# Performance work log

Hardware: AMD Instinct MI355X
Metric: run time of the kernel (lower is better)

The kernel has to match this reference:

```python
import jax, jax.numpy as jnp
import numpy as np

DELTA = 5.0  # HuberLoss delta from the torch module


def setup_inputs() -> dict:
    key = jax.random.key(0)
    k1, k2 = jax.random.split(key)
    shape = (8, 1, 160, 160, 160)
    return {
        "y_pred_logits": jax.random.normal(k1, shape, dtype=jnp.float32),
        "y_true": jax.random.normal(k2, shape, dtype=jnp.float32),
    }


def reference(y_pred_logits, y_true):
    bs = y_true.shape[0]
    pred = y_pred_logits.astype(jnp.float32).reshape(bs, -1)
    true = y_true.astype(jnp.float32).reshape(bs, -1)
    e = pred - true
    ae = jnp.abs(e)
    # per-sample mean losses (matches per-iteration nn.MSELoss / L1Loss / HuberLoss)
    L2 = jnp.mean(e * e, axis=1)
    L1 = jnp.mean(ae, axis=1)
    huber_elem = jnp.where(ae <= DELTA, 0.5 * e * e, DELTA * (ae - 0.5 * DELTA))
    huber = jnp.mean(huber_elem, axis=1)
    # branch logic: L2 if (L2 <= 1) or (L2 > 1 and L2 < L1**2), else huber
    use_l2 = (L2 <= 1.0) | (L2 < L1 * L1)
    per_sample = jnp.where(use_l2, L2, huber)
    return jnp.mean(per_sample)
```

## Files before the change

### kernel.cpp

```cpp
#include <hip/hip_runtime.h>


#define TPB 256
#define BPS 500
constexpr int    F4_PER_SAMPLE = 1024000;
constexpr int    F4_PER_BLOCK  = 2048;
constexpr double PER_SAMPLE_D  = 4096000.0;
constexpr float  DELTA = 5.0f;

typedef float vf4 __attribute__((ext_vector_type(4)));

__global__ __launch_bounds__(TPB, 4) void adap_stage1(
    const vf4* __restrict__ pred,
    const vf4* __restrict__ truth,
    float* __restrict__ part)
{
    const int s   = blockIdx.y;
    const int b   = blockIdx.x;
    const int tid = threadIdx.x;
    const int base = s * F4_PER_SAMPLE + b * F4_PER_BLOCK + tid;

    vf4 p[8], t[8];
    #pragma unroll
    for (int j = 0; j < 8; ++j) {
        p[j] = pred [base + j * TPB];
        t[j] = truth[base + j * TPB];
    }

    float sum2 = 0.0f, sum1 = 0.0f, sumh = 0.0f;
    #pragma unroll
    for (int j = 0; j < 8; ++j) {
        float e0 = p[j].x - t[j].x, e1 = p[j].y - t[j].y;
        float e2 = p[j].z - t[j].z, e3 = p[j].w - t[j].w;
        float a0 = fabsf(e0), a1 = fabsf(e1), a2 = fabsf(e2), a3 = fabsf(e3);

        sum2 += e0*e0 + e1*e1 + e2*e2 + e3*e3;
        sum1 += a0 + a1 + a2 + a3;

        float h0 = (a0 <= DELTA) ? 0.5f*e0*e0 : DELTA*(a0 - 0.5f*DELTA);
        float h1 = (a1 <= DELTA) ? 0.5f*e1*e1 : DELTA*(a1 - 0.5f*DELTA);
        float h2 = (a2 <= DELTA) ? 0.5f*e2*e2 : DELTA*(a2 - 0.5f*DELTA);
        float h3 = (a3 <= DELTA) ? 0.5f*e3*e3 : DELTA*(a3 - 0.5f*DELTA);
        sumh += h0 + h1 + h2 + h3;
    }

    #pragma unroll
    for (int off = 32; off > 0; off >>= 1) {
        sum2 += __shfl_down(sum2, off, 64);
        sum1 += __shfl_down(sum1, off, 64);
        sumh += __shfl_down(sumh, off, 64);
    }

    __shared__ float w2[4], w1[4], wh[4];
    const int wave = tid >> 6, lane = tid & 63;
    if (lane == 0) { w2[wave] = sum2; w1[wave] = sum1; wh[wave] = sumh; }
    __syncthreads();
    if (tid == 0) {
        float a = 0.f, c = 0.f, h = 0.f;
        #pragma unroll
        for (int w = 0; w < 4; ++w) { a += w2[w]; c += w1[w]; h += wh[w]; }
        const int o = (s * BPS + b) * 3;
        part[o + 0] = a;
        part[o + 1] = c;
        part[o + 2] = h;
    }
}

__global__ __launch_bounds__(TPB) void adap_stage2(
    const float* __restrict__ part,
    float* __restrict__ out)
{
    const int tid  = threadIdx.x;
    const int s    = tid >> 5;
    const int lane = tid & 31;

    double a = 0.0, b = 0.0, h = 0.0;
    for (int k = lane; k < BPS; k += 32) {
        const float* p = part + (s * BPS + k) * 3;
        a += (double)p[0];
        b += (double)p[1];
        h += (double)p[2];
    }
    #pragma unroll
    for (int off = 16; off > 0; off >>= 1) {
        a += __shfl_down(a, off, 32);
        b += __shfl_down(b, off, 32);
        h += __shfl_down(h, off, 32);
    }

    __shared__ double ps[8];
    if (lane == 0) {
        const double inv = 1.0 / PER_SAMPLE_D;
        double L2 = a * inv, L1 = b * inv, H = h * inv;
        bool use_l2 = (L2 <= 1.0) || (L2 < L1 * L1);
        ps[s] = use_l2 ? L2 : H;
    }
    __syncthreads();
    if (tid == 0) {
        double acc = 0.0;
        #pragma unroll
        for (int i = 0; i < 8; ++i) acc += ps[i];
        out[0] = (float)(acc * 0.125);
    }
}

extern "C" void kernel_launch(void* const* d_in, const int* in_sizes, int n_in,
                              void* d_out, int out_size, void* d_ws, size_t ws_size,
                              hipStream_t stream) {
    const vf4* pred  = (const vf4*)d_in[0];
    const vf4* truth = (const vf4*)d_in[1];
    float* part = (float*)d_ws;
    float* out  = (float*)d_out;

    dim3 grid1(BPS, 8);
    adap_stage1<<<grid1, TPB, 0, stream>>>(pred, truth, part);
    adap_stage2<<<1, TPB, 0, stream>>>(part, out);
}
```

Baseline: 274.1 us.

## Stream inputs through LDS with double-buffered async global_load_lds per wave

```diff
diff --git a/kernel.cpp b/kernel.cpp
--- a/kernel.cpp
+++ b/kernel.cpp
@@ -2,46 +2,78 @@
 
 
 #define TPB 256
-#define BPS 500
-constexpr int    F4_PER_SAMPLE = 1024000;
-constexpr int    F4_PER_BLOCK  = 2048;
-constexpr double PER_SAMPLE_D  = 4096000.0;
+#define BPS 250
+constexpr int    FLOATS_PER_SAMPLE = 4096000;
+constexpr int    F_PER_BLOCK = 16384;
+constexpr int    F_PER_WAVE  = 4096;
+constexpr int    F_PER_ITER  = 512;
+constexpr int    ITERS       = 8;
+constexpr double PER_SAMPLE_D = 4096000.0;
 constexpr float  DELTA = 5.0f;
 
 typedef float vf4 __attribute__((ext_vector_type(4)));
+#define AS1 __attribute__((address_space(1)))
+#define AS3 __attribute__((address_space(3)))
 
 __global__ __launch_bounds__(TPB, 4) void adap_stage1(
-    const vf4* __restrict__ pred,
-    const vf4* __restrict__ truth,
+    const float* __restrict__ pred,
+    const float* __restrict__ truth,
     float* __restrict__ part)
 {
-    const int s   = blockIdx.y;
-    const int b   = blockIdx.x;
-    const int tid = threadIdx.x;
-    const int base = s * F4_PER_SAMPLE + b * F4_PER_BLOCK + tid;
+    const int s    = blockIdx.y;
+    const int b    = blockIdx.x;
+    const int tid  = threadIdx.x;
+    const int w    = tid >> 6;
+    const int lane = tid & 63;
 
-    vf4 p[8], t[8];
-    #pragma unroll
-    for (int j = 0; j < 8; ++j) {
-        p[j] = pred [base + j * TPB];
-        t[j] = truth[base + j * TPB];
-    }
+    __shared__ float lds[2][4][2][F_PER_ITER];
+
+    const float* pbase = pred  + s * FLOATS_PER_SAMPLE + b * F_PER_BLOCK + w * F_PER_WAVE;
+    const float* tbase = truth + s * FLOATS_PER_SAMPLE + b * F_PER_BLOCK + w * F_PER_WAVE;
+
+    auto stage = [&](int bf, int it) {
+        const float* gp = pbase + it * F_PER_ITER + lane * 4;
+        const float* gt = tbase + it * F_PER_ITER + lane * 4;
+        __builtin_amdgcn_global_load_lds((AS1 const void*)gp,         (AS3 void*)&lds[bf][w][0][0],   16, 0, 0);
+        __builtin_amdgcn_global_load_lds((AS1 const void*)(gp + 256), (AS3 void*)&lds[bf][w][0][256], 16, 0, 0);
+        __builtin_amdgcn_global_load_lds((AS1 const void*)gt,         (AS3 void*)&lds[bf][w][1][0],   16, 0, 0);
+        __builtin_amdgcn_global_load_lds((AS1 const void*)(gt + 256), (AS3 void*)&lds[bf][w][1][256], 16, 0, 0);
+    };
 
     float sum2 = 0.0f, sum1 = 0.0f, sumh = 0.0f;
+
+    stage(0, 0);
     #pragma unroll
-    for (int j = 0; j < 8; ++j) {
-        float e0 = p[j].x - t[j].x, e1 = p[j].y - t[j].y;
-        float e2 = p[j].z - t[j].z, e3 = p[j].w - t[j].w;
-        float a0 = fabsf(e0), a1 = fabsf(e1), a2 = fabsf(e2), a3 = fabsf(e3);
+    for (int it = 0; it < ITERS; ++it) {
+        const int bf = it & 1;
+        if (it + 1 < ITERS) {
+            stage(bf ^ 1, it + 1);
+            asm volatile("s_waitcnt vmcnt(4)" ::: "memory");
+        } else {
+            asm volatile("s_waitcnt vmcnt(0)" ::: "memory");
+        }
 
-        sum2 += e0*e0 + e1*e1 + e2*e2 + e3*e3;
-        sum1 += a0 + a1 + a2 + a3;
+        const vf4* lp = (const vf4*)&lds[bf][w][0][0];
+        const vf4* lt = (const vf4*)&lds[bf][w][1][0];
+        vf4 pv[2], tv[2];
+        pv[0] = lp[lane]; pv[1] = lp[lane + 64];
+        tv[0] = lt[lane]; tv[1] = lt[lane + 64];
 
-        float h0 = (a0 <= DELTA) ? 0.5f*e0*e0 : DELTA*(a0 - 0.5f*DELTA);
-        float h1 = (a1 <= DELTA) ? 0.5f*e1*e1 : DELTA*(a1 - 0.5f*DELTA);
-        float h2 = (a2 <= DELTA) ? 0.5f*e2*e2 : DELTA*(a2 - 0.5f*DELTA);
-        float h3 = (a3 <= DELTA) ? 0.5f*e3*e3 : DELTA*(a3 - 0.5f*DELTA);
-        sumh += h0 + h1 + h2 + h3;
+        #pragma unroll
+        for (int j = 0; j < 2; ++j) {
+            float e0 = pv[j].x - tv[j].x, e1 = pv[j].y - tv[j].y;
+            float e2 = pv[j].z - tv[j].z, e3 = pv[j].w - tv[j].w;
+            float a0 = fabsf(e0), a1 = fabsf(e1), a2 = fabsf(e2), a3 = fabsf(e3);
+
+            sum2 += e0*e0 + e1*e1 + e2*e2 + e3*e3;
+            sum1 += a0 + a1 + a2 + a3;
+
+            float h0 = (a0 <= DELTA) ? 0.5f*e0*e0 : DELTA*(a0 - 0.5f*DELTA);
+            float h1 = (a1 <= DELTA) ? 0.5f*e1*e1 : DELTA*(a1 - 0.5f*DELTA);
+            float h2 = (a2 <= DELTA) ? 0.5f*e2*e2 : DELTA*(a2 - 0.5f*DELTA);
+            float h3 = (a3 <= DELTA) ? 0.5f*e3*e3 : DELTA*(a3 - 0.5f*DELTA);
+            sumh += h0 + h1 + h2 + h3;
+        }
     }
 
     #pragma unroll
@@ -52,13 +84,12 @@
     }
 
     __shared__ float w2[4], w1[4], wh[4];
-    const int wave = tid >> 6, lane = tid & 63;
-    if (lane == 0) { w2[wave] = sum2; w1[wave] = sum1; wh[wave] = sumh; }
+    if (lane == 0) { w2[w] = sum2; w1[w] = sum1; wh[w] = sumh; }
     __syncthreads();
     if (tid == 0) {
         float a = 0.f, c = 0.f, h = 0.f;
         #pragma unroll
-        for (int w = 0; w < 4; ++w) { a += w2[w]; c += w1[w]; h += wh[w]; }
+        for (int q = 0; q < 4; ++q) { a += w2[q]; c += w1[q]; h += wh[q]; }
         const int o = (s * BPS + b) * 3;
         part[o + 0] = a;
         part[o + 1] = c;
@@ -107,8 +138,8 @@
 extern "C" void kernel_launch(void* const* d_in, const int* in_sizes, int n_in,
                               void* d_out, int out_size, void* d_ws, size_t ws_size,
                               hipStream_t stream) {
-    const vf4* pred  = (const vf4*)d_in[0];
-    const vf4* truth = (const vf4*)d_in[1];
+    const float* pred  = (const float*)d_in[0];
+    const float* truth = (const float*)d_in[1];
     float* part = (float*)d_ws;
     float* out  = (float*)d_out;
 
```

New measurement: 270.9 us. About the same (-1.2%).
